# Kernel optimization log

Hardware: AMD Instinct MI355X
Metric: run time of the kernel (lower is better)

## Reference

```python
import jax, jax.numpy as jnp
import numpy as np

N = 8192          # mesh vertices
E = 49152         # directed edges (avg degree 6)
M = 25            # kernel_size per pseudo-dim
DIM = 3           # pseudo-coordinate dim
K = M ** DIM      # 15625 weight matrices per layer
S = 2 ** DIM      # 8 nonzero degree-1 B-spline products per edge
LC, UC = -0.22703196, 0.36853024   # curvature range
LM, UM = 1.2585511, 1.648841       # myelin range
R = 10.0
LAYER_DIMS = [(2, 32), (32, 64), (64, 64), (64, 32), (32, 1)]


def transform(x):
    # rescale curv/myelin channels into [-R, R] with clamping (matches torch masking)
    t0 = (x[:, 0] - LC) / (UC - LC) * (2.0 * R) - R
    t1 = (x[:, 1] - LM) / (UM - LM) * (2.0 * R) - R
    return jnp.stack([jnp.clip(t0, -R, R), jnp.clip(t1, -R, R)], axis=1)


def spline_basis(pseudo):
    # open B-spline, degree 1: v in [0, M-1); 8 corner products per edge
    v = pseudo * (M - 1)
    lo = jnp.floor(v)
    f = v - lo                                                    # [E, DIM]
    lo = lo.astype(jnp.int32)
    bits = (jnp.arange(S)[:, None] >> jnp.arange(DIM)[None, :]) & 1   # [S, DIM]
    oh = bits.astype(pseudo.dtype)
    basis = jnp.prod(oh[None] * f[:, None, :] + (1.0 - oh[None]) * (1.0 - f[:, None, :]), axis=-1)  # [E, S]
    strides = (M ** jnp.arange(DIM)).astype(jnp.int32)
    wi = jnp.sum((lo[:, None, :] + bits[None]) * strides[None, None, :], axis=-1)  # [E, S] kernel indices
    return basis, wi


def spline_conv(h, src, dst, basis, wi, W, root, bias):
    xj = h[src]                                             # [E, Fin] gather
    msg = jnp.zeros((xj.shape[0], W.shape[2]), h.dtype)
    for s in range(S):                                      # fixed 8-way basis loop
        msg = msg + basis[:, s, None] * jnp.einsum('ei,eio->eo', xj, W[wi[:, s]])
    agg = jax.ops.segment_sum(msg, dst, num_segments=N)     # scatter-sum (norm=False)
    return agg + h @ root + bias


def setup_inputs() -> dict:
    key = jax.random.key(0)
    ks = jax.random.split(key, 3 + 2 * len(LAYER_DIMS))
    inp = {
        "x": jax.random.normal(ks[0], (N, 2), dtype=jnp.float32),
        "edge_index": jax.random.randint(ks[1], (2, E), 0, N),
        "pseudo": jax.random.uniform(ks[2], (E, DIM), dtype=jnp.float32),
    }
    for i, (fi, fo) in enumerate(LAYER_DIMS):
        kw, kr = ks[3 + 2 * i], ks[4 + 2 * i]
        inp[f"W{i+1}"] = jax.random.normal(kw, (K, fi, fo), dtype=jnp.float32) / np.float32(np.sqrt(fi * S))
        inp[f"root{i+1}"] = jax.random.normal(kr, (fi, fo), dtype=jnp.float32) / np.float32(np.sqrt(fi))
        inp[f"b{i+1}"] = jnp.zeros((fo,), dtype=jnp.float32)
    return inp


def reference(x, edge_index, pseudo, W1, root1, b1, W2, root2, b2, W3, root3, b3,
              W4, root4, b4, W5, root5, b5):
    src, dst = edge_index[0], edge_index[1]
    basis, wi = spline_basis(pseudo)   # shared across all 5 layers, as in the torch model
    h = transform(x)
    for W, r, b in ((W1, root1, b1), (W2, root2, b2), (W3, root3, b3),
                    (W4, root4, b4), (W5, root5, b5)):
        h = jax.nn.elu(spline_conv(h, src, dst, basis, wi, W, r, b))
    return h.reshape(-1)
```

## Files before the change

### kernel.cpp

```cpp
#include <hip/hip_runtime.h>
#include <math.h>

#define NV 8192
#define EV 49152
#define KK 15625

__device__ __forceinline__ void edge_frac(const float* __restrict__ pseudo, int e,
                                          float f[3], int lo[3]) {
#pragma unroll
    for (int j = 0; j < 3; ++j) {
        float v = pseudo[e * 3 + j] * 24.0f;
        float fl = floorf(v);
        int l = (int)fl;
        l = l < 0 ? 0 : (l > 23 ? 23 : l);
        lo[j] = l;
        f[j] = v - (float)l;
    }
}

__global__ void transform_kernel(const float* __restrict__ x, float* __restrict__ h0) {
    int n = blockIdx.x * blockDim.x + threadIdx.x;
    if (n >= NV) return;
    const float LC = -0.22703196f, UC = 0.36853024f;
    const float LM = 1.2585511f, UM = 1.648841f;
    const float R = 10.0f;
    float t0 = (x[n * 2 + 0] - LC) / (UC - LC) * (2.0f * R) - R;
    float t1 = (x[n * 2 + 1] - LM) / (UM - LM) * (2.0f * R) - R;
    h0[n * 2 + 0] = fminf(fmaxf(t0, -R), R);
    h0[n * 2 + 1] = fminf(fmaxf(t1, -R), R);
}

__global__ void hist_kernel(const float* __restrict__ pseudo, int* __restrict__ counts) {
    int e = blockIdx.x * blockDim.x + threadIdx.x;
    if (e >= EV) return;
    float f[3]; int lo[3];
    edge_frac(pseudo, e, f, lo);
#pragma unroll
    for (int s = 0; s < 8; ++s) {
        int wi = (lo[0] + (s & 1)) + 25 * (lo[1] + ((s >> 1) & 1)) + 625 * (lo[2] + ((s >> 2) & 1));
        atomicAdd(&counts[wi], 1);
    }
}

__global__ void scan_kernel(const int* __restrict__ counts, int* __restrict__ offsets,
                            int* __restrict__ cursor) {
    __shared__ int sums[256];
    const int CH = 62;
    int t = threadIdx.x;
    int base = t * CH;
    int s = 0;
    for (int i = 0; i < CH; ++i) {
        int idx = base + i;
        if (idx < KK) s += counts[idx];
    }
    sums[t] = s;
    __syncthreads();
    for (int d = 1; d < 256; d <<= 1) {
        int v = (t >= d) ? sums[t - d] : 0;
        __syncthreads();
        sums[t] += v;
        __syncthreads();
    }
    int run = (t > 0) ? sums[t - 1] : 0;
    for (int i = 0; i < CH; ++i) {
        int idx = base + i;
        if (idx < KK) {
            offsets[idx] = run;
            cursor[idx] = run;
            run += counts[idx];
        }
    }
    if (t == 255) offsets[KK] = run;
}

__global__ void scatter_kernel(const float* __restrict__ pseudo, int* __restrict__ cursor,
                               int* __restrict__ pair_e, float* __restrict__ pair_b) {
    int e = blockIdx.x * blockDim.x + threadIdx.x;
    if (e >= EV) return;
    float f[3]; int lo[3];
    edge_frac(pseudo, e, f, lo);
#pragma unroll
    for (int s = 0; s < 8; ++s) {
        float b = ((s & 1) ? f[0] : 1.0f - f[0]) *
                  (((s >> 1) & 1) ? f[1] : 1.0f - f[1]) *
                  (((s >> 2) & 1) ? f[2] : 1.0f - f[2]);
        int wi = (lo[0] + (s & 1)) + 25 * (lo[1] + ((s >> 1) & 1)) + 625 * (lo[2] + ((s >> 2) & 1));
        int pos = atomicAdd(&cursor[wi], 1);
        pair_e[pos] = e;
        pair_b[pos] = b;
    }
}

template <int FIN, int FOUT>
__global__ __launch_bounds__(64) void conv_kernel(
    const float* __restrict__ h, const float* __restrict__ W,
    const int* __restrict__ offsets, const int* __restrict__ pair_e,
    const float* __restrict__ pair_b, const int* __restrict__ ei,
    float* __restrict__ agg) {
    constexpr int PPI = 64 / FOUT;
    int k = blockIdx.x;
    int start = offsets[k], end = offsets[k + 1];
    if (start >= end) return;
    int lane = threadIdx.x;
    int g = lane / FOUT;
    int o = lane % FOUT;
    const float* Wk = W + (size_t)k * (FIN * FOUT);
    float w[FIN];
#pragma unroll
    for (int i = 0; i < FIN; ++i) w[i] = Wk[i * FOUT + o];
    __shared__ float xsh[PPI][FIN];
    for (int p = start; p < end; p += PPI) {
        int pp = p + g;
        bool valid = (pp < end);
        int psafe = valid ? pp : start;
        int e = pair_e[psafe];
        float b = valid ? pair_b[psafe] : 0.0f;
        int src = ei[e];
        int dst = ei[EV + e];
        __syncthreads();
        for (int i = o; i < FIN; i += FOUT) xsh[g][i] = h[src * FIN + i];
        __syncthreads();
        float acc = 0.0f;
#pragma unroll
        for (int i = 0; i < FIN; ++i) acc += xsh[g][i] * w[i];
        if (valid) atomicAdd(&agg[(size_t)dst * FOUT + o], b * acc);
    }
}

__global__ __launch_bounds__(64) void conv_kernel_f1(
    const float* __restrict__ h, const float* __restrict__ W,
    const int* __restrict__ offsets, const int* __restrict__ pair_e,
    const float* __restrict__ pair_b, const int* __restrict__ ei,
    float* __restrict__ agg) {
    int k = blockIdx.x;
    int start = offsets[k], end = offsets[k + 1];
    if (start >= end) return;
    int lane = threadIdx.x;
    const float* Wk = W + (size_t)k * 32;
    float w[32];
#pragma unroll
    for (int i = 0; i < 32; ++i) w[i] = Wk[i];
    for (int pp = start + lane; pp < end; pp += 64) {
        int e = pair_e[pp];
        float b = pair_b[pp];
        int src = ei[e];
        int dst = ei[EV + e];
        float acc = 0.0f;
#pragma unroll
        for (int i = 0; i < 32; ++i) acc += h[src * 32 + i] * w[i];
        atomicAdd(&agg[dst], b * acc);
    }
}

template <int FIN, int FOUT>
__global__ void node_kernel(const float* __restrict__ h, const float* __restrict__ agg,
                            const float* __restrict__ root, const float* __restrict__ bias,
                            float* __restrict__ hout) {
    int idx = blockIdx.x * blockDim.x + threadIdx.x;
    if (idx >= NV * FOUT) return;
    int n = idx / FOUT, o = idx % FOUT;
    float acc = agg[idx] + bias[o];
#pragma unroll
    for (int i = 0; i < FIN; ++i) acc += h[n * FIN + i] * root[i * FOUT + o];
    hout[idx] = acc > 0.0f ? acc : expm1f(acc);
}

extern "C" void kernel_launch(void* const* d_in, const int* in_sizes, int n_in,
                              void* d_out, int out_size, void* d_ws, size_t ws_size,
                              hipStream_t stream) {
    const float* x      = (const float*)d_in[0];
    const int*   ei     = (const int*)d_in[1];
    const float* pseudo = (const float*)d_in[2];
    const float* W1 = (const float*)d_in[3];
    const float* r1 = (const float*)d_in[4];
    const float* b1 = (const float*)d_in[5];
    const float* W2 = (const float*)d_in[6];
    const float* r2 = (const float*)d_in[7];
    const float* b2 = (const float*)d_in[8];
    const float* W3 = (const float*)d_in[9];
    const float* r3 = (const float*)d_in[10];
    const float* b3 = (const float*)d_in[11];
    const float* W4 = (const float*)d_in[12];
    const float* r4 = (const float*)d_in[13];
    const float* b4 = (const float*)d_in[14];
    const float* W5 = (const float*)d_in[15];
    const float* r5 = (const float*)d_in[16];
    const float* b5 = (const float*)d_in[17];

    char* ws = (char*)d_ws;
    size_t off = 0;
    auto alloc = [&](size_t bytes) {
        void* p = ws + off;
        off += (bytes + 255) & ~(size_t)255;
        return p;
    };
    int*   counts  = (int*)alloc(KK * sizeof(int));
    int*   offsets = (int*)alloc((KK + 1) * sizeof(int));
    int*   cursor  = (int*)alloc(KK * sizeof(int));
    int*   pair_e  = (int*)alloc((size_t)EV * 8 * sizeof(int));
    float* pair_b  = (float*)alloc((size_t)EV * 8 * sizeof(float));
    float* hA      = (float*)alloc((size_t)NV * 64 * sizeof(float));
    float* hB      = (float*)alloc((size_t)NV * 64 * sizeof(float));
    float* agg     = (float*)alloc((size_t)NV * 64 * sizeof(float));

    hipMemsetAsync(counts, 0, KK * sizeof(int), stream);
    transform_kernel<<<(NV + 255) / 256, 256, 0, stream>>>(x, hA);
    hist_kernel<<<(EV + 255) / 256, 256, 0, stream>>>(pseudo, counts);
    scan_kernel<<<1, 256, 0, stream>>>(counts, offsets, cursor);
    scatter_kernel<<<(EV + 255) / 256, 256, 0, stream>>>(pseudo, cursor, pair_e, pair_b);

    hipMemsetAsync(agg, 0, (size_t)NV * 32 * sizeof(float), stream);
    conv_kernel<2, 32><<<KK, 64, 0, stream>>>(hA, W1, offsets, pair_e, pair_b, ei, agg);
    node_kernel<2, 32><<<(NV * 32 + 255) / 256, 256, 0, stream>>>(hA, agg, r1, b1, hB);

    hipMemsetAsync(agg, 0, (size_t)NV * 64 * sizeof(float), stream);
    conv_kernel<32, 64><<<KK, 64, 0, stream>>>(hB, W2, offsets, pair_e, pair_b, ei, agg);
    node_kernel<32, 64><<<(NV * 64 + 255) / 256, 256, 0, stream>>>(hB, agg, r2, b2, hA);

    hipMemsetAsync(agg, 0, (size_t)NV * 64 * sizeof(float), stream);
    conv_kernel<64, 64><<<KK, 64, 0, stream>>>(hA, W3, offsets, pair_e, pair_b, ei, agg);
    node_kernel<64, 64><<<(NV * 64 + 255) / 256, 256, 0, stream>>>(hA, agg, r3, b3, hB);

    hipMemsetAsync(agg, 0, (size_t)NV * 32 * sizeof(float), stream);
    conv_kernel<64, 32><<<KK, 64, 0, stream>>>(hB, W4, offsets, pair_e, pair_b, ei, agg);
    node_kernel<64, 32><<<(NV * 32 + 255) / 256, 256, 0, stream>>>(hB, agg, r4, b4, hA);

    hipMemsetAsync(agg, 0, (size_t)NV * sizeof(float), stream);
    conv_kernel_f1<<<KK, 64, 0, stream>>>(hA, W5, offsets, pair_e, pair_b, ei, agg);
    node_kernel<32, 1><<<(NV + 255) / 256, 256, 0, stream>>>(hA, agg, r5, b5, (float*)d_out);
}
```

Measured before the change: 612.2 us.

## Use 4-wave blocks per weight bucket with float4 gathers and wave barriers

The per-kernel-index conv kernels now launch 256 threads, so four wavefronts process disjoint pairs of the same weight bucket. Each wave has its own shared-memory slot and syncs with wave barriers instead of block-wide __syncthreads. Source features are gathered as float4 and the dot product is split across four accumulators. Layer 1 gets a dedicated kernel that reads the two input features directly. Buckets average about 25 pairs, so most extra waves may sit idle, and each wave redundantly loads the weights into registers.

```diff
diff --git a/kernel.cpp b/kernel.cpp
--- a/kernel.cpp
+++ b/kernel.cpp
@@ -92,38 +92,79 @@
 }
 
 template <int FIN, int FOUT>
-__global__ __launch_bounds__(64) void conv_kernel(
+__global__ __launch_bounds__(256) void conv_v2(
     const float* __restrict__ h, const float* __restrict__ W,
     const int* __restrict__ offsets, const int* __restrict__ pair_e,
     const float* __restrict__ pair_b, const int* __restrict__ ei,
     float* __restrict__ agg) {
     constexpr int PPI = 64 / FOUT;
+    constexpr int STRIDE = 4 * PPI;
+    constexpr int NL4 = FIN / 4;
     int k = blockIdx.x;
     int start = offsets[k], end = offsets[k + 1];
     if (start >= end) return;
-    int lane = threadIdx.x;
+    int t = threadIdx.x;
+    int w = t >> 6;
+    int lane = t & 63;
     int g = lane / FOUT;
     int o = lane % FOUT;
     const float* Wk = W + (size_t)k * (FIN * FOUT);
-    float w[FIN];
-#pragma unroll
-    for (int i = 0; i < FIN; ++i) w[i] = Wk[i * FOUT + o];
-    __shared__ float xsh[PPI][FIN];
-    for (int p = start; p < end; p += PPI) {
-        int pp = p + g;
+    float wreg[FIN];
+#pragma unroll
+    for (int i = 0; i < FIN; ++i) wreg[i] = Wk[i * FOUT + o];
+    __shared__ float4 xsh[4][PPI][NL4];
+
+    for (int p0 = start + w * PPI; p0 < end; p0 += STRIDE) {
+        int pp = p0 + g;
         bool valid = (pp < end);
         int psafe = valid ? pp : start;
         int e = pair_e[psafe];
-        float b = valid ? pair_b[psafe] : 0.0f;
+        float b = pair_b[psafe];
         int src = ei[e];
         int dst = ei[EV + e];
-        __syncthreads();
-        for (int i = o; i < FIN; i += FOUT) xsh[g][i] = h[src * FIN + i];
-        __syncthreads();
-        float acc = 0.0f;
-#pragma unroll
-        for (int i = 0; i < FIN; ++i) acc += xsh[g][i] * w[i];
-        if (valid) atomicAdd(&agg[(size_t)dst * FOUT + o], b * acc);
+        if (o < NL4) xsh[w][g][o] = ((const float4*)h)[(size_t)src * NL4 + o];
+        __builtin_amdgcn_wave_barrier();
+        float a0 = 0.0f, a1 = 0.0f, a2 = 0.0f, a3 = 0.0f;
+#pragma unroll
+        for (int i4 = 0; i4 < NL4; ++i4) {
+            float4 xv = xsh[w][g][i4];
+            a0 += xv.x * wreg[4 * i4 + 0];
+            a1 += xv.y * wreg[4 * i4 + 1];
+            a2 += xv.z * wreg[4 * i4 + 2];
+            a3 += xv.w * wreg[4 * i4 + 3];
+        }
+        __builtin_amdgcn_wave_barrier();
+        if (valid) atomicAdd(&agg[(size_t)dst * FOUT + o], b * ((a0 + a1) + (a2 + a3)));
+    }
+}
+
+__global__ __launch_bounds__(256) void conv_l1(
+    const float* __restrict__ h, const float* __restrict__ W,
+    const int* __restrict__ offsets, const int* __restrict__ pair_e,
+    const float* __restrict__ pair_b, const int* __restrict__ ei,
+    float* __restrict__ agg) {
+    constexpr int FOUT = 32, PPI = 2, STRIDE = 8;
+    int k = blockIdx.x;
+    int start = offsets[k], end = offsets[k + 1];
+    if (start >= end) return;
+    int t = threadIdx.x;
+    int w = t >> 6;
+    int lane = t & 63;
+    int g = lane / FOUT;
+    int o = lane % FOUT;
+    const float* Wk = W + (size_t)k * 64;
+    float w0 = Wk[o], w1 = Wk[32 + o];
+    for (int p0 = start + w * PPI; p0 < end; p0 += STRIDE) {
+        int pp = p0 + g;
+        bool valid = (pp < end);
+        int psafe = valid ? pp : start;
+        int e = pair_e[psafe];
+        float b = pair_b[psafe];
+        int src = ei[e];
+        int dst = ei[EV + e];
+        float x0 = h[src * 2 + 0];
+        float x1 = h[src * 2 + 1];
+        if (valid) atomicAdd(&agg[(size_t)dst * FOUT + o], b * (x0 * w0 + x1 * w1));
     }
 }
 
@@ -210,19 +251,19 @@
     scatter_kernel<<<(EV + 255) / 256, 256, 0, stream>>>(pseudo, cursor, pair_e, pair_b);
 
     hipMemsetAsync(agg, 0, (size_t)NV * 32 * sizeof(float), stream);
-    conv_kernel<2, 32><<<KK, 64, 0, stream>>>(hA, W1, offsets, pair_e, pair_b, ei, agg);
+    conv_l1<<<KK, 256, 0, stream>>>(hA, W1, offsets, pair_e, pair_b, ei, agg);
     node_kernel<2, 32><<<(NV * 32 + 255) / 256, 256, 0, stream>>>(hA, agg, r1, b1, hB);
 
     hipMemsetAsync(agg, 0, (size_t)NV * 64 * sizeof(float), stream);
-    conv_kernel<32, 64><<<KK, 64, 0, stream>>>(hB, W2, offsets, pair_e, pair_b, ei, agg);
+    conv_v2<32, 64><<<KK, 256, 0, stream>>>(hB, W2, offsets, pair_e, pair_b, ei, agg);
     node_kernel<32, 64><<<(NV * 64 + 255) / 256, 256, 0, stream>>>(hB, agg, r2, b2, hA);
 
     hipMemsetAsync(agg, 0, (size_t)NV * 64 * sizeof(float), stream);
-    conv_kernel<64, 64><<<KK, 64, 0, stream>>>(hA, W3, offsets, pair_e, pair_b, ei, agg);
+    conv_v2<64, 64><<<KK, 256, 0, stream>>>(hA, W3, offsets, pair_e, pair_b, ei, agg);
     node_kernel<64, 64><<<(NV * 64 + 255) / 256, 256, 0, stream>>>(hA, agg, r3, b3, hB);
 
     hipMemsetAsync(agg, 0, (size_t)NV * 32 * sizeof(float), stream);
-    conv_kernel<64, 32><<<KK, 64, 0, stream>>>(hB, W4, offsets, pair_e, pair_b, ei, agg);
+    conv_v2<64, 32><<<KK, 256, 0, stream>>>(hB, W4, offsets, pair_e, pair_b, ei, agg);
     node_kernel<64, 32><<<(NV * 32 + 255) / 256, 256, 0, stream>>>(hB, agg, r4, b4, hA);
 
     hipMemsetAsync(agg, 0, (size_t)NV * sizeof(float), stream);
```

New measurement: 611.2 us. Within noise of the previous version (-0.2%).

## Precompute src/dst per pair and pipeline float4 feature panels in conv kernels

Applied to the files above, without the earlier changes.

The scatter kernel now stores the source index and basis weight packed together, plus the destination, so conv kernels no longer do a dependent lookup through edge_index. Conv kernels handle four weight matrices per 256-thread block, one per wave. They load gathered feature rows as float4, pre-scale them by the basis weight, and double-buffer 16-pair panels in shared memory with wave barriers instead of block-wide syncthreads. Layer 1 and the final layer get specialised kernels, the last using shuffle reductions. The cost is more register pressure from float4 panels and weight registers, and more shared memory per block.

```diff
diff --git a/kernel.cpp b/kernel.cpp
--- a/kernel.cpp
+++ b/kernel.cpp
@@ -73,12 +73,15 @@
     if (t == 255) offsets[KK] = run;
 }
 
-__global__ void scatter_kernel(const float* __restrict__ pseudo, int* __restrict__ cursor,
-                               int* __restrict__ pair_e, float* __restrict__ pair_b) {
+__global__ void scatter_kernel(const float* __restrict__ pseudo, const int* __restrict__ ei,
+                               int* __restrict__ cursor,
+                               int2* __restrict__ pair_sb, int* __restrict__ pair_dst) {
     int e = blockIdx.x * blockDim.x + threadIdx.x;
     if (e >= EV) return;
     float f[3]; int lo[3];
     edge_frac(pseudo, e, f, lo);
+    int src = ei[e];
+    int dst = ei[EV + e];
 #pragma unroll
     for (int s = 0; s < 8; ++s) {
         float b = ((s & 1) ? f[0] : 1.0f - f[0]) *
@@ -86,69 +89,133 @@
                   (((s >> 2) & 1) ? f[2] : 1.0f - f[2]);
         int wi = (lo[0] + (s & 1)) + 25 * (lo[1] + ((s >> 1) & 1)) + 625 * (lo[2] + ((s >> 2) & 1));
         int pos = atomicAdd(&cursor[wi], 1);
-        pair_e[pos] = e;
-        pair_b[pos] = b;
+        pair_sb[pos] = make_int2(src, __float_as_int(b));
+        pair_dst[pos] = dst;
     }
 }
 
 template <int FIN, int FOUT>
-__global__ __launch_bounds__(64) void conv_kernel(
+__global__ __launch_bounds__(256) void conv_v3(
     const float* __restrict__ h, const float* __restrict__ W,
-    const int* __restrict__ offsets, const int* __restrict__ pair_e,
-    const float* __restrict__ pair_b, const int* __restrict__ ei,
-    float* __restrict__ agg) {
-    constexpr int PPI = 64 / FOUT;
-    int k = blockIdx.x;
-    int start = offsets[k], end = offsets[k + 1];
-    if (start >= end) return;
-    int lane = threadIdx.x;
+    const int* __restrict__ offsets, const int2* __restrict__ pair_sb,
+    const int* __restrict__ pair_dst, float* __restrict__ agg) {
+    constexpr int P = 16;
+    constexpr int C4 = FIN / 4;
+    constexpr int J = C4 / 4;
+    constexpr int RG = 64 / FOUT;
+    int w = threadIdx.x >> 6;
+    int lane = threadIdx.x & 63;
+    int k = blockIdx.x * 4 + w;
+    if (k >= KK) return;
+    int start = offsets[k];
+    int n = offsets[k + 1] - start;
+    if (n <= 0) return;
+    int o = lane % FOUT;
     int g = lane / FOUT;
-    int o = lane % FOUT;
     const float* Wk = W + (size_t)k * (FIN * FOUT);
-    float w[FIN];
-#pragma unroll
-    for (int i = 0; i < FIN; ++i) w[i] = Wk[i * FOUT + o];
-    __shared__ float xsh[PPI][FIN];
-    for (int p = start; p < end; p += PPI) {
-        int pp = p + g;
-        bool valid = (pp < end);
-        int psafe = valid ? pp : start;
-        int e = pair_e[psafe];
-        float b = valid ? pair_b[psafe] : 0.0f;
-        int src = ei[e];
-        int dst = ei[EV + e];
-        __syncthreads();
-        for (int i = o; i < FIN; i += FOUT) xsh[g][i] = h[src * FIN + i];
-        __syncthreads();
-        float acc = 0.0f;
-#pragma unroll
-        for (int i = 0; i < FIN; ++i) acc += xsh[g][i] * w[i];
-        if (valid) atomicAdd(&agg[(size_t)dst * FOUT + o], b * acc);
-    }
-}
-
-__global__ __launch_bounds__(64) void conv_kernel_f1(
+    float wreg[FIN];
+#pragma unroll
+    for (int i = 0; i < FIN; ++i) wreg[i] = Wk[i * FOUT + o];
+
+    __shared__ float4 xsh[4][2][P][C4];
+    int sr = lane >> 2;
+    int sc = lane & 3;
+
+    const float4* h4 = (const float4*)h;
+
+    float4 v[J];
+    auto ldpanel = [&](int p0) {
+        int pp = p0 + sr;
+        int2 sb = (pp < n) ? pair_sb[start + pp] : make_int2(0, 0);
+        float b = __int_as_float(sb.y);
+        const float4* hr = h4 + (size_t)sb.x * C4;
+#pragma unroll
+        for (int j = 0; j < J; ++j) {
+            float4 t = hr[sc + 4 * j];
+            v[j] = make_float4(t.x * b, t.y * b, t.z * b, t.w * b);
+        }
+    };
+    auto stpanel = [&](int buf) {
+#pragma unroll
+        for (int j = 0; j < J; ++j) xsh[w][buf][sr][sc + 4 * j] = v[j];
+    };
+    auto cpanel = [&](int buf, int p0) {
+        int lim = n - p0;
+        if (lim > P) lim = P;
+        for (int r = g; r < lim; r += RG) {
+            int dst = pair_dst[start + p0 + r];
+            float a0 = 0.0f, a1 = 0.0f, a2 = 0.0f, a3 = 0.0f;
+#pragma unroll
+            for (int i4 = 0; i4 < C4; ++i4) {
+                float4 xv = xsh[w][buf][r][i4];
+                a0 += xv.x * wreg[4 * i4 + 0];
+                a1 += xv.y * wreg[4 * i4 + 1];
+                a2 += xv.z * wreg[4 * i4 + 2];
+                a3 += xv.w * wreg[4 * i4 + 3];
+            }
+            atomicAdd(&agg[(size_t)dst * FOUT + o], (a0 + a1) + (a2 + a3));
+        }
+    };
+
+    int nP = (n + P - 1) / P;
+    ldpanel(0);
+    stpanel(0);
+    for (int p = 0; p < nP; ++p) {
+        int buf = p & 1;
+        if (p + 1 < nP) ldpanel((p + 1) * P);
+        cpanel(buf, p * P);
+        if (p + 1 < nP) stpanel(buf ^ 1);
+        __builtin_amdgcn_wave_barrier();
+    }
+}
+
+__global__ __launch_bounds__(256) void conv_l1(
     const float* __restrict__ h, const float* __restrict__ W,
-    const int* __restrict__ offsets, const int* __restrict__ pair_e,
-    const float* __restrict__ pair_b, const int* __restrict__ ei,
-    float* __restrict__ agg) {
-    int k = blockIdx.x;
-    int start = offsets[k], end = offsets[k + 1];
-    if (start >= end) return;
-    int lane = threadIdx.x;
-    const float* Wk = W + (size_t)k * 32;
-    float w[32];
-#pragma unroll
-    for (int i = 0; i < 32; ++i) w[i] = Wk[i];
-    for (int pp = start + lane; pp < end; pp += 64) {
-        int e = pair_e[pp];
-        float b = pair_b[pp];
-        int src = ei[e];
-        int dst = ei[EV + e];
-        float acc = 0.0f;
-#pragma unroll
-        for (int i = 0; i < 32; ++i) acc += h[src * 32 + i] * w[i];
-        atomicAdd(&agg[dst], b * acc);
+    const int* __restrict__ offsets, const int2* __restrict__ pair_sb,
+    const int* __restrict__ pair_dst, float* __restrict__ agg) {
+    int w = threadIdx.x >> 6;
+    int lane = threadIdx.x & 63;
+    int k = blockIdx.x * 4 + w;
+    if (k >= KK) return;
+    int start = offsets[k];
+    int n = offsets[k + 1] - start;
+    if (n <= 0) return;
+    int o = lane & 31;
+    int g = lane >> 5;
+    const float* Wk = W + (size_t)k * 64;
+    float w0 = Wk[o], w1 = Wk[32 + o];
+    const float2* h2 = (const float2*)h;
+    for (int r = g; r < n; r += 2) {
+        int2 sb = pair_sb[start + r];
+        float b = __int_as_float(sb.y);
+        int dst = pair_dst[start + r];
+        float2 xv = h2[sb.x];
+        atomicAdd(&agg[(size_t)dst * 32 + o], b * (xv.x * w0 + xv.y * w1));
+    }
+}
+
+__global__ __launch_bounds__(256) void conv_f1(
+    const float* __restrict__ h, const float* __restrict__ W,
+    const int* __restrict__ offsets, const int2* __restrict__ pair_sb,
+    const int* __restrict__ pair_dst, float* __restrict__ agg) {
+    int w = threadIdx.x >> 6;
+    int lane = threadIdx.x & 63;
+    int k = blockIdx.x * 4 + w;
+    if (k >= KK) return;
+    int start = offsets[k];
+    int n = offsets[k + 1] - start;
+    if (n <= 0) return;
+    int i = lane & 31;
+    int g = lane >> 5;
+    float wk = W[(size_t)k * 32 + i];
+    for (int r = g; r < n; r += 2) {
+        int2 sb = pair_sb[start + r];
+        float b = __int_as_float(sb.y);
+        int dst = pair_dst[start + r];
+        float val = h[(size_t)sb.x * 32 + i] * wk * b;
+#pragma unroll
+        for (int d = 16; d >= 1; d >>= 1) val += __shfl_xor(val, d, 32);
+        if (i == 0) atomicAdd(&agg[dst], val);
     }
 }
 
@@ -194,38 +261,40 @@
         off += (bytes + 255) & ~(size_t)255;
         return p;
     };
-    int*   counts  = (int*)alloc(KK * sizeof(int));
-    int*   offsets = (int*)alloc((KK + 1) * sizeof(int));
-    int*   cursor  = (int*)alloc(KK * sizeof(int));
-    int*   pair_e  = (int*)alloc((size_t)EV * 8 * sizeof(int));
-    float* pair_b  = (float*)alloc((size_t)EV * 8 * sizeof(float));
-    float* hA      = (float*)alloc((size_t)NV * 64 * sizeof(float));
-    float* hB      = (float*)alloc((size_t)NV * 64 * sizeof(float));
-    float* agg     = (float*)alloc((size_t)NV * 64 * sizeof(float));
+    int*   counts   = (int*)alloc(KK * sizeof(int));
+    int*   offsets  = (int*)alloc((KK + 1) * sizeof(int));
+    int*   cursor   = (int*)alloc(KK * sizeof(int));
+    int2*  pair_sb  = (int2*)alloc((size_t)EV * 8 * sizeof(int2));
+    int*   pair_dst = (int*)alloc((size_t)EV * 8 * sizeof(int));
+    float* hA       = (float*)alloc((size_t)NV * 64 * sizeof(float));
+    float* hB       = (float*)alloc((size_t)NV * 64 * sizeof(float));
+    float* agg      = (float*)alloc((size_t)NV * 64 * sizeof(float));
+
+    const int CGRID = (KK + 3) / 4;
 
     hipMemsetAsync(counts, 0, KK * sizeof(int), stream);
     transform_kernel<<<(NV + 255) / 256, 256, 0, stream>>>(x, hA);
     hist_kernel<<<(EV + 255) / 256, 256, 0, stream>>>(pseudo, counts);
     scan_kernel<<<1, 256, 0, stream>>>(counts, offsets, cursor);
-    scatter_kernel<<<(EV + 255) / 256, 256, 0, stream>>>(pseudo, cursor, pair_e, pair_b);
+    scatter_kernel<<<(EV + 255) / 256, 256, 0, stream>>>(pseudo, ei, cursor, pair_sb, pair_dst);
 
     hipMemsetAsync(agg, 0, (size_t)NV * 32 * sizeof(float), stream);
-    conv_kernel<2, 32><<<KK, 64, 0, stream>>>(hA, W1, offsets, pair_e, pair_b, ei, agg);
+    conv_l1<<<CGRID, 256, 0, stream>>>(hA, W1, offsets, pair_sb, pair_dst, agg);
     node_kernel<2, 32><<<(NV * 32 + 255) / 256, 256, 0, stream>>>(hA, agg, r1, b1, hB);
 
     hipMemsetAsync(agg, 0, (size_t)NV * 64 * sizeof(float), stream);
-    conv_kernel<32, 64><<<KK, 64, 0, stream>>>(hB, W2, offsets, pair_e, pair_b, ei, agg);
+    conv_v3<32, 64><<<CGRID, 256, 0, stream>>>(hB, W2, offsets, pair_sb, pair_dst, agg);
     node_kernel<32, 64><<<(NV * 64 + 255) / 256, 256, 0, stream>>>(hB, agg, r2, b2, hA);
 
     hipMemsetAsync(agg, 0, (size_t)NV * 64 * sizeof(float), stream);
-    conv_kernel<64, 64><<<KK, 64, 0, stream>>>(hA, W3, offsets, pair_e, pair_b, ei, agg);
+    conv_v3<64, 64><<<CGRID, 256, 0, stream>>>(hA, W3, offsets, pair_sb, pair_dst, agg);
     node_kernel<64, 64><<<(NV * 64 + 255) / 256, 256, 0, stream>>>(hA, agg, r3, b3, hB);
 
     hipMemsetAsync(agg, 0, (size_t)NV * 32 * sizeof(float), stream);
-    conv_kernel<64, 32><<<KK, 64, 0, stream>>>(hB, W4, offsets, pair_e, pair_b, ei, agg);
+    conv_v3<64, 32><<<CGRID, 256, 0, stream>>>(hB, W4, offsets, pair_sb, pair_dst, agg);
     node_kernel<64, 32><<<(NV * 32 + 255) / 256, 256, 0, stream>>>(hB, agg, r4, b4, hA);
 
     hipMemsetAsync(agg, 0, (size_t)NV * sizeof(float), stream);
-    conv_kernel_f1<<<KK, 64, 0, stream>>>(hA, W5, offsets, pair_e, pair_b, ei, agg);
+    conv_f1<<<CGRID, 256, 0, stream>>>(hA, W5, offsets, pair_sb, pair_dst, agg);
     node_kernel<32, 1><<<(NV + 255) / 256, 256, 0, stream>>>(hA, agg, r5, b5, (float*)d_out);
 }
```

Result: faster. 515.9 us (-15.7%).
